# Optimization experiments

Hardware: AMD Instinct MI355X
Metric: run time of the kernel (lower is better)

The kernel has to match this reference:

```python
import jax, jax.numpy as jnp
import numpy as np

B, S, D = 8, 2048, 768

def setup_inputs() -> dict:
    key = jax.random.key(0)
    kx, kq, kk, kv = jax.random.split(key, 4)
    scale = 1.0 / np.sqrt(D)
    x = jax.random.normal(kx, (B, S, D), dtype=jnp.float32)
    # nn.Linear weights: [out, in], applied as x @ W.T
    Wq = jax.random.normal(kq, (D, D), dtype=jnp.float32) * scale
    Wk = jax.random.normal(kk, (D, D), dtype=jnp.float32) * scale
    Wv = jax.random.normal(kv, (D, D), dtype=jnp.float32) * scale
    return {"x": x, "Wq": Wq, "Wk": Wk, "Wv": Wv}

def reference(x, Wq, Wk, Wv):
    d_k = x.shape[-1]
    Q = jnp.einsum('bsd,ed->bse', x, Wq)
    K = jnp.einsum('bsd,ed->bse', x, Wk)
    V = jnp.einsum('bsd,ed->bse', x, Wv)
    scores = jnp.einsum('bqd,bkd->bqk', Q, K) / jnp.sqrt(jnp.float32(d_k))
    attention_weights = jax.nn.softmax(scores, axis=-1)  # [B,S,S]
    weighted_values = jnp.einsum('bqk,bkd->bqd', attention_weights, V)
    return (weighted_values, attention_weights)
```

## Files before the change

kernel.cpp:

```cpp
#include <hip/hip_runtime.h>
#include <cmath>


typedef __bf16 v8bf __attribute__((ext_vector_type(8)));
typedef float  v4f  __attribute__((ext_vector_type(4)));
typedef unsigned short u16;

__device__ __forceinline__ u16 f2bf(float f) {
  union { float f; unsigned u; } v; v.f = f;
  unsigned r = v.u + 0x7fffu + ((v.u >> 16) & 1u);
  return (u16)(r >> 16);
}

__device__ __forceinline__ uint4 pack8(const float* __restrict__ src) {
  float4 f0 = *(const float4*)src;
  float4 f1 = *(const float4*)(src + 4);
  union { uint4 u; u16 h[8]; } pk;
  pk.h[0] = f2bf(f0.x); pk.h[1] = f2bf(f0.y); pk.h[2] = f2bf(f0.z); pk.h[3] = f2bf(f0.w);
  pk.h[4] = f2bf(f1.x); pk.h[5] = f2bf(f1.y); pk.h[6] = f2bf(f1.z); pk.h[7] = f2bf(f1.w);
  return pk.u;
}

__device__ __forceinline__ void gl_lds16(const void* g, void* l) {
  __builtin_amdgcn_global_load_lds(
      (const __attribute__((address_space(1))) unsigned*)g,
      (__attribute__((address_space(3))) unsigned*)l, 16, 0, 0);
}

enum { OUT_F32 = 0, OUT_BF16 = 1, OUT_VT_BF16 = 2 };

constexpr int BM = 128, BN = 128, BK = 64;

template <bool A_F32, int MODE>
__global__ __launch_bounds__(256)
void gemm128(const void* __restrict__ Ag_, const void* __restrict__ Bg_,
             void* __restrict__ Cg, int K, int lda, int ldb, int ldc,
             long long sA, long long sB, long long sC, float alpha) {
  __shared__ u16 As[BM * BK];
  __shared__ u16 Bs[BN * BK];

  const int z  = blockIdx.z;
  const int m0 = blockIdx.x * BM;
  const int n0 = blockIdx.y * BN;

  const int t    = threadIdx.x;
  const int lane = t & 63;
  const int w    = t >> 6;
  const int wm   = (w & 1) * 64;
  const int wn   = (w >> 1) * 64;
  const int fr   = lane & 15;
  const int quad = lane >> 4;

  const u16* Bp = (const u16*)Bg_ + (size_t)z * (size_t)sB;

  v4f acc[4][4];
#pragma unroll
  for (int i = 0; i < 4; ++i)
#pragma unroll
    for (int j = 0; j < 4; ++j) acc[i][j] = (v4f){0.f, 0.f, 0.f, 0.f};

  for (int kt = 0; kt < K; kt += BK) {
#pragma unroll
    for (int j = 0; j < 4; ++j) {
      const int s   = (w * 4 + j) * 64 + lane;
      const int row = s >> 3;
      const int gc  = (s & 7) ^ (row & 7);
      gl_lds16(Bp + (size_t)(n0 + row) * ldb + kt + gc * 8, &Bs[s * 8]);
    }
    if constexpr (A_F32) {
      const float* Ap = (const float*)Ag_ + (size_t)z * (size_t)sA;
#pragma unroll
      for (int j = 0; j < 4; ++j) {
        const int g   = j * 256 + t;
        const int row = g >> 3, gc = g & 7;
        const int s   = (g & ~7) | (gc ^ (row & 7));
        uint4 pk = pack8(Ap + (size_t)(m0 + row) * lda + kt + gc * 8);
        *(uint4*)&As[s * 8] = pk;
      }
    } else {
      const u16* Ap = (const u16*)Ag_ + (size_t)z * (size_t)sA;
#pragma unroll
      for (int j = 0; j < 4; ++j) {
        const int s   = (w * 4 + j) * 64 + lane;
        const int row = s >> 3;
        const int gc  = (s & 7) ^ (row & 7);
        gl_lds16(Ap + (size_t)(m0 + row) * lda + kt + gc * 8, &As[s * 8]);
      }
    }
    __syncthreads();

#pragma unroll
    for (int kk = 0; kk < BK; kk += 32) {
      const int kc = (kk >> 3) + quad;
      v8bf af[4], bv[4];
#pragma unroll
      for (int i = 0; i < 4; ++i) {
        const int ra = wm + i * 16 + fr;
        const int rb = wn + i * 16 + fr;
        af[i] = *(const v8bf*)&As[(ra * 8 + (kc ^ (fr & 7))) * 8];
        bv[i] = *(const v8bf*)&Bs[(rb * 8 + (kc ^ (fr & 7))) * 8];
      }
#pragma unroll
      for (int mi = 0; mi < 4; ++mi)
#pragma unroll
        for (int ni = 0; ni < 4; ++ni)
          acc[mi][ni] =
              __builtin_amdgcn_mfma_f32_16x16x32_bf16(af[mi], bv[ni], acc[mi][ni], 0, 0, 0);
    }
    __syncthreads();
  }

  const int r0 = (lane >> 4) * 4;
#pragma unroll
  for (int mi = 0; mi < 4; ++mi) {
#pragma unroll
    for (int ni = 0; ni < 4; ++ni) {
      v4f v = acc[mi][ni];
      const int grow0 = m0 + wm + mi * 16 + r0;
      const int gcol  = n0 + wn + ni * 16 + fr;
      if constexpr (MODE == OUT_F32) {
        float* C = (float*)Cg + (size_t)z * (size_t)sC;
#pragma unroll
        for (int r = 0; r < 4; ++r)
          C[(size_t)(grow0 + r) * ldc + gcol] = v[r] * alpha;
      } else if constexpr (MODE == OUT_BF16) {
        u16* C = (u16*)Cg;
#pragma unroll
        for (int r = 0; r < 4; ++r)
          C[(size_t)(grow0 + r) * ldc + gcol] = f2bf(v[r]);
      } else {
        u16* C = (u16*)Cg;
        size_t base = (size_t)(grow0 >> 11) * (768ull * 2048ull) +
                      (size_t)gcol * 2048ull + (size_t)(grow0 & 2047);
        ushort4 st;
        st.x = f2bf(v[0]); st.y = f2bf(v[1]); st.z = f2bf(v[2]); st.w = f2bf(v[3]);
        *(ushort4*)&C[base] = st;
      }
    }
  }
}

__global__ __launch_bounds__(256)
void cvt_bf16(const float* __restrict__ src, u16* __restrict__ dst, int n8) {
  const int i = blockIdx.x * 256 + threadIdx.x;
  if (i < n8) *(uint4*)(dst + (size_t)i * 8) = pack8(src + (size_t)i * 8);
}

__global__ __launch_bounds__(256)
void cvt3_bf16(const float* __restrict__ s0, const float* __restrict__ s1,
               const float* __restrict__ s2, u16* __restrict__ d0,
               u16* __restrict__ d1, u16* __restrict__ d2, int n8) {
  const float* s = blockIdx.y == 0 ? s0 : blockIdx.y == 1 ? s1 : s2;
  u16*         d = blockIdx.y == 0 ? d0 : blockIdx.y == 1 ? d1 : d2;
  const int i = blockIdx.x * 256 + threadIdx.x;
  if (i < n8) *(uint4*)(d + (size_t)i * 8) = pack8(s + (size_t)i * 8);
}

template <bool EMIT>
__global__ __launch_bounds__(256) void softmax_rows(float* __restrict__ w,
                                                    u16* __restrict__ pb) {
  float* p = w + (size_t)blockIdx.x * 2048;
  const int t = threadIdx.x;
  float4 a = *(float4*)(p + t * 4);
  float4 b = *(float4*)(p + 1024 + t * 4);

  float mx = fmaxf(fmaxf(fmaxf(a.x, a.y), fmaxf(a.z, a.w)),
                   fmaxf(fmaxf(b.x, b.y), fmaxf(b.z, b.w)));
#pragma unroll
  for (int off = 32; off; off >>= 1) mx = fmaxf(mx, __shfl_xor(mx, off));
  __shared__ float red[4];
  const int wid = t >> 6, ln = t & 63;
  if (ln == 0) red[wid] = mx;
  __syncthreads();
  mx = fmaxf(fmaxf(red[0], red[1]), fmaxf(red[2], red[3]));

  a.x = __expf(a.x - mx); a.y = __expf(a.y - mx);
  a.z = __expf(a.z - mx); a.w = __expf(a.w - mx);
  b.x = __expf(b.x - mx); b.y = __expf(b.y - mx);
  b.z = __expf(b.z - mx); b.w = __expf(b.w - mx);

  float s = a.x + a.y + a.z + a.w + b.x + b.y + b.z + b.w;
#pragma unroll
  for (int off = 32; off; off >>= 1) s += __shfl_xor(s, off);
  __syncthreads();
  if (ln == 0) red[wid] = s;
  __syncthreads();
  s = red[0] + red[1] + red[2] + red[3];

  const float inv = 1.0f / s;
  a.x *= inv; a.y *= inv; a.z *= inv; a.w *= inv;
  b.x *= inv; b.y *= inv; b.z *= inv; b.w *= inv;
  *(float4*)(p + t * 4) = a;
  *(float4*)(p + 1024 + t * 4) = b;

  if constexpr (EMIT) {
    u16* q = pb + (size_t)blockIdx.x * 2048;
    ushort4 ha, hb;
    ha.x = f2bf(a.x); ha.y = f2bf(a.y); ha.z = f2bf(a.z); ha.w = f2bf(a.w);
    hb.x = f2bf(b.x); hb.y = f2bf(b.y); hb.z = f2bf(b.z); hb.w = f2bf(b.w);
    *(ushort4*)(q + t * 4) = ha;
    *(ushort4*)(q + 1024 + t * 4) = hb;
  }
}

extern "C" void kernel_launch(void* const* d_in, const int* in_sizes, int n_in,
                              void* d_out, int out_size, void* d_ws, size_t ws_size,
                              hipStream_t stream) {
  const float* x  = (const float*)d_in[0];
  const float* Wq = (const float*)d_in[1];
  const float* Wk = (const float*)d_in[2];
  const float* Wv = (const float*)d_in[3];
  float* out = (float*)d_out;
  float* wts = out + 8ull * 2048 * 768;

  u16* Qb  = (u16*)d_out;
  u16* Kb  = Qb + 16384ull * 768;
  u16* xb  = (u16*)wts;
  u16* Wqb = xb + 16384ull * 768;
  u16* Wkb = Wqb + 768ull * 768;
  u16* Wvb = Wkb + 768ull * 768;
  u16* Vt  = (u16*)d_ws;
  u16* Pb  = Vt + 8ull * 768 * 2048;

  const size_t VT_BYTES = 8ull * 768 * 2048 * 2;
  const size_t PB_BYTES = 8ull * 2048 * 2048 * 2;
  const bool   pb_ok    = ws_size >= VT_BYTES + PB_BYTES;

  const dim3 blk(256, 1, 1);
  const float isq = 1.0f / sqrtf(768.0f);

  cvt_bf16<<<dim3(6144, 1, 1), blk, 0, stream>>>(x, xb, 16384 * 768 / 8);
  cvt3_bf16<<<dim3(288, 3, 1), blk, 0, stream>>>(Wq, Wk, Wv, Wqb, Wkb, Wvb,
                                                 768 * 768 / 8);

  gemm128<false, OUT_BF16><<<dim3(128, 6, 1), blk, 0, stream>>>(
      xb, Wqb, (void*)Qb, 768, 768, 768, 768, 0, 0, 0, 1.0f);
  gemm128<false, OUT_BF16><<<dim3(128, 6, 1), blk, 0, stream>>>(
      xb, Wkb, (void*)Kb, 768, 768, 768, 768, 0, 0, 0, 1.0f);
  gemm128<false, OUT_VT_BF16><<<dim3(128, 6, 1), blk, 0, stream>>>(
      xb, Wvb, (void*)Vt, 768, 768, 768, 0, 0, 0, 0, 1.0f);

  gemm128<false, OUT_F32><<<dim3(16, 16, 8), blk, 0, stream>>>(
      Qb, Kb, (void*)wts, 768, 768, 768, 2048,
      2048ll * 768, 2048ll * 768, 2048ll * 2048, isq);

  if (pb_ok) {
    softmax_rows<true><<<dim3(16384, 1, 1), blk, 0, stream>>>(wts, Pb);
    gemm128<false, OUT_F32><<<dim3(16, 6, 8), blk, 0, stream>>>(
        Pb, Vt, (void*)out, 2048, 2048, 2048, 768,
        2048ll * 2048, 768ll * 2048, 2048ll * 768, 1.0f);
  } else {
    softmax_rows<false><<<dim3(16384, 1, 1), blk, 0, stream>>>(wts, nullptr);
    gemm128<true, OUT_F32><<<dim3(16, 6, 8), blk, 0, stream>>>(
        wts, Vt, (void*)out, 2048, 2048, 2048, 768,
        2048ll * 2048, 768ll * 2048, 2048ll * 768, 1.0f);
  }
}
```

Before: 462.1 us.

## Add 256x256 MFMA GEMM kernel and fuse Q/K/V projections into one launch

Adds a 512-thread GEMM kernel with 256x256 tiles, a 64-wide K step, XOR-swizzled LDS staging via global_load_lds, and a workgroup-index remap that groups blocks in strides of eight. The three projection GEMMs become a single launch over the contiguous Wq/Wk/Wv bf16 buffers, with the epilogue routing each column group to Q, K or the transposed V layout. The QK^T score GEMM also moves to the larger tile. The aim is more data reuse per block and fewer launches, at the cost of higher register and LDS pressure, no double buffering, and fewer blocks in flight.

```diff
diff --git a/kernel.cpp b/kernel.cpp
--- a/kernel.cpp
+++ b/kernel.cpp
@@ -140,6 +140,130 @@
   }
 }
 
+enum { S_F32 = 0, S_QKV = 1 };
+constexpr int BM2 = 256, BN2 = 256, BK2 = 64;
+
+template <int MODE>
+__global__ __launch_bounds__(512, 2)
+void gemm256(const u16* __restrict__ Ag, const u16* __restrict__ Bg,
+             void* __restrict__ C0, void* __restrict__ C1, void* __restrict__ C2,
+             int K, int lda, int ldb, int ldc,
+             long long sA, long long sB, long long sC, float alpha) {
+  __shared__ u16 As[BM2 * BK2];
+  __shared__ u16 Bs[BN2 * BK2];
+
+  const int gx = gridDim.x, gy = gridDim.y, gz = gridDim.z;
+  const int nwg = gx * gy * gz;
+  int lid = blockIdx.x + gx * (blockIdx.y + gy * blockIdx.z);
+  if ((nwg & 7) == 0) {
+    const int cpx = nwg >> 3;
+    lid = (lid & 7) * cpx + (lid >> 3);
+  }
+  const int bx = lid % gx;
+  const int byz = lid / gx;
+  const int by = byz % gy;
+  const int z  = byz / gy;
+
+  const int m0 = bx * BM2;
+  const int n0 = by * BN2;
+
+  const int t    = threadIdx.x;
+  const int lane = t & 63;
+  const int w    = t >> 6;
+  const int wm   = (w >> 2) * 128;
+  const int wn   = (w & 3) * 64;
+  const int fr   = lane & 15;
+  const int quad = lane >> 4;
+
+  const u16* Ap = Ag + (size_t)z * (size_t)sA;
+  const u16* Bp = Bg + (size_t)z * (size_t)sB;
+
+  v4f acc[8][4];
+#pragma unroll
+  for (int i = 0; i < 8; ++i)
+#pragma unroll
+    for (int j = 0; j < 4; ++j) acc[i][j] = (v4f){0.f, 0.f, 0.f, 0.f};
+
+  for (int kt = 0; kt < K; kt += BK2) {
+#pragma unroll
+    for (int j = 0; j < 4; ++j) {
+      const int s   = (w * 4 + j) * 64 + lane;
+      const int row = s >> 3;
+      const int gc  = (s & 7) ^ (row & 7);
+      gl_lds16(Bp + (size_t)(n0 + row) * ldb + kt + gc * 8, &Bs[s * 8]);
+    }
+#pragma unroll
+    for (int j = 0; j < 4; ++j) {
+      const int s   = (w * 4 + j) * 64 + lane;
+      const int row = s >> 3;
+      const int gc  = (s & 7) ^ (row & 7);
+      gl_lds16(Ap + (size_t)(m0 + row) * lda + kt + gc * 8, &As[s * 8]);
+    }
+    __syncthreads();
+
+#pragma unroll
+    for (int kk = 0; kk < BK2; kk += 32) {
+      const int kc = (kk >> 3) + quad;
+      v8bf af[8], bv[4];
+#pragma unroll
+      for (int i = 0; i < 8; ++i) {
+        const int ra = wm + i * 16 + fr;
+        af[i] = *(const v8bf*)&As[(ra * 8 + (kc ^ (fr & 7))) * 8];
+      }
+#pragma unroll
+      for (int i = 0; i < 4; ++i) {
+        const int rb = wn + i * 16 + fr;
+        bv[i] = *(const v8bf*)&Bs[(rb * 8 + (kc ^ (fr & 7))) * 8];
+      }
+#pragma unroll
+      for (int mi = 0; mi < 8; ++mi)
+#pragma unroll
+        for (int ni = 0; ni < 4; ++ni)
+          acc[mi][ni] =
+              __builtin_amdgcn_mfma_f32_16x16x32_bf16(af[mi], bv[ni], acc[mi][ni], 0, 0, 0);
+    }
+    __syncthreads();
+  }
+
+  const int r0 = (lane >> 4) * 4;
+#pragma unroll
+  for (int mi = 0; mi < 8; ++mi) {
+#pragma unroll
+    for (int ni = 0; ni < 4; ++ni) {
+      v4f v = acc[mi][ni];
+      const int grow0 = m0 + wm + mi * 16 + r0;
+      const int gcol  = n0 + wn + ni * 16 + fr;
+      if constexpr (MODE == S_F32) {
+        float* C = (float*)C0 + (size_t)z * (size_t)sC;
+#pragma unroll
+        for (int r = 0; r < 4; ++r)
+          C[(size_t)(grow0 + r) * ldc + gcol] = v[r] * alpha;
+      } else {
+        const int grp  = n0 / 768;
+        const int lcol = gcol - grp * 768;
+        if (grp == 0) {
+          u16* C = (u16*)C0;
+#pragma unroll
+          for (int r = 0; r < 4; ++r)
+            C[(size_t)(grow0 + r) * 768 + lcol] = f2bf(v[r]);
+        } else if (grp == 1) {
+          u16* C = (u16*)C1;
+#pragma unroll
+          for (int r = 0; r < 4; ++r)
+            C[(size_t)(grow0 + r) * 768 + lcol] = f2bf(v[r]);
+        } else {
+          u16* C = (u16*)C2;
+          size_t base = (size_t)(grow0 >> 11) * (768ull * 2048ull) +
+                        (size_t)lcol * 2048ull + (size_t)(grow0 & 2047);
+          ushort4 st;
+          st.x = f2bf(v[0]); st.y = f2bf(v[1]); st.z = f2bf(v[2]); st.w = f2bf(v[3]);
+          *(ushort4*)&C[base] = st;
+        }
+      }
+    }
+  }
+}
+
 __global__ __launch_bounds__(256)
 void cvt_bf16(const float* __restrict__ src, u16* __restrict__ dst, int n8) {
   const int i = blockIdx.x * 256 + threadIdx.x;
@@ -227,21 +351,18 @@
   const bool   pb_ok    = ws_size >= VT_BYTES + PB_BYTES;
 
   const dim3 blk(256, 1, 1);
+  const dim3 blk512(512, 1, 1);
   const float isq = 1.0f / sqrtf(768.0f);
 
   cvt_bf16<<<dim3(6144, 1, 1), blk, 0, stream>>>(x, xb, 16384 * 768 / 8);
   cvt3_bf16<<<dim3(288, 3, 1), blk, 0, stream>>>(Wq, Wk, Wv, Wqb, Wkb, Wvb,
                                                  768 * 768 / 8);
 
-  gemm128<false, OUT_BF16><<<dim3(128, 6, 1), blk, 0, stream>>>(
-      xb, Wqb, (void*)Qb, 768, 768, 768, 768, 0, 0, 0, 1.0f);
-  gemm128<false, OUT_BF16><<<dim3(128, 6, 1), blk, 0, stream>>>(
-      xb, Wkb, (void*)Kb, 768, 768, 768, 768, 0, 0, 0, 1.0f);
-  gemm128<false, OUT_VT_BF16><<<dim3(128, 6, 1), blk, 0, stream>>>(
-      xb, Wvb, (void*)Vt, 768, 768, 768, 0, 0, 0, 0, 1.0f);
-
-  gemm128<false, OUT_F32><<<dim3(16, 16, 8), blk, 0, stream>>>(
-      Qb, Kb, (void*)wts, 768, 768, 768, 2048,
+  gemm256<S_QKV><<<dim3(64, 9, 1), blk512, 0, stream>>>(
+      xb, Wqb, (void*)Qb, (void*)Kb, (void*)Vt, 768, 768, 768, 0, 0, 0, 0, 1.0f);
+
+  gemm256<S_F32><<<dim3(8, 8, 8), blk512, 0, stream>>>(
+      Qb, Kb, (void*)wts, nullptr, nullptr, 768, 768, 768, 2048,
       2048ll * 768, 2048ll * 768, 2048ll * 2048, isq);
 
   if (pb_ok) {
```

Measured after the change: 491.5 us. 6.4% more time.

## Double-buffer GEMM LDS tiles and fuse Q/K/V projections into one launch

Applied to the files above, without the earlier changes.

The GEMM kernel now keeps two LDS buffers for the A and B tiles. It issues the global-to-LDS loads for the next K tile before running the MFMA work on the current one, so memory latency overlaps with compute and one barrier per iteration is dropped. The three projection GEMMs become a single launch with 18 column-block groups. It relies on the bf16 Wq/Wk/Wv buffers being contiguous and routes each group's output to Q, K or transposed V. The cost is double the LDS per block, which may reduce occupancy, and some branching in the epilogue.

```diff
diff --git a/kernel.cpp b/kernel.cpp
--- a/kernel.cpp
+++ b/kernel.cpp
@@ -27,17 +27,19 @@
       (__attribute__((address_space(3))) unsigned*)l, 16, 0, 0);
 }
 
-enum { OUT_F32 = 0, OUT_BF16 = 1, OUT_VT_BF16 = 2 };
+enum { OUT_F32 = 0, OUT_QKV = 1 };
 
 constexpr int BM = 128, BN = 128, BK = 64;
+constexpr int TILE = BM * BK;
 
 template <bool A_F32, int MODE>
 __global__ __launch_bounds__(256)
 void gemm128(const void* __restrict__ Ag_, const void* __restrict__ Bg_,
-             void* __restrict__ Cg, int K, int lda, int ldb, int ldc,
+             void* __restrict__ C0, void* __restrict__ C1, void* __restrict__ C2,
+             int K, int lda, int ldb, int ldc,
              long long sA, long long sB, long long sC, float alpha) {
-  __shared__ u16 As[BM * BK];
-  __shared__ u16 Bs[BN * BK];
+  __shared__ u16 As[2 * TILE];
+  __shared__ u16 Bs[2 * TILE];
 
   const int z  = blockIdx.z;
   const int m0 = blockIdx.x * BM;
@@ -59,13 +61,14 @@
 #pragma unroll
     for (int j = 0; j < 4; ++j) acc[i][j] = (v4f){0.f, 0.f, 0.f, 0.f};
 
-  for (int kt = 0; kt < K; kt += BK) {
+  auto stage = [&](int kt, int buf) {
 #pragma unroll
     for (int j = 0; j < 4; ++j) {
       const int s   = (w * 4 + j) * 64 + lane;
       const int row = s >> 3;
       const int gc  = (s & 7) ^ (row & 7);
-      gl_lds16(Bp + (size_t)(n0 + row) * ldb + kt + gc * 8, &Bs[s * 8]);
+      gl_lds16(Bp + (size_t)(n0 + row) * ldb + kt + gc * 8,
+               &Bs[buf * TILE + s * 8]);
     }
     if constexpr (A_F32) {
       const float* Ap = (const float*)Ag_ + (size_t)z * (size_t)sA;
@@ -75,7 +78,7 @@
         const int row = g >> 3, gc = g & 7;
         const int s   = (g & ~7) | (gc ^ (row & 7));
         uint4 pk = pack8(Ap + (size_t)(m0 + row) * lda + kt + gc * 8);
-        *(uint4*)&As[s * 8] = pk;
+        *(uint4*)&As[buf * TILE + s * 8] = pk;
       }
     } else {
       const u16* Ap = (const u16*)Ag_ + (size_t)z * (size_t)sA;
@@ -84,11 +87,21 @@
         const int s   = (w * 4 + j) * 64 + lane;
         const int row = s >> 3;
         const int gc  = (s & 7) ^ (row & 7);
-        gl_lds16(Ap + (size_t)(m0 + row) * lda + kt + gc * 8, &As[s * 8]);
-      }
-    }
-    __syncthreads();
-
+        gl_lds16(Ap + (size_t)(m0 + row) * lda + kt + gc * 8,
+                 &As[buf * TILE + s * 8]);
+      }
+    }
+  };
+
+  stage(0, 0);
+  __syncthreads();
+
+  int cur = 0;
+  for (int kt = 0; kt < K; kt += BK) {
+    if (kt + BK < K) stage(kt + BK, cur ^ 1);
+
+    const u16* Ab = &As[cur * TILE];
+    const u16* Bb = &Bs[cur * TILE];
 #pragma unroll
     for (int kk = 0; kk < BK; kk += 32) {
       const int kc = (kk >> 3) + quad;
@@ -97,8 +110,8 @@
       for (int i = 0; i < 4; ++i) {
         const int ra = wm + i * 16 + fr;
         const int rb = wn + i * 16 + fr;
-        af[i] = *(const v8bf*)&As[(ra * 8 + (kc ^ (fr & 7))) * 8];
-        bv[i] = *(const v8bf*)&Bs[(rb * 8 + (kc ^ (fr & 7))) * 8];
+        af[i] = *(const v8bf*)&Ab[(ra * 8 + (kc ^ (fr & 7))) * 8];
+        bv[i] = *(const v8bf*)&Bb[(rb * 8 + (kc ^ (fr & 7))) * 8];
       }
 #pragma unroll
       for (int mi = 0; mi < 4; ++mi)
@@ -108,6 +121,7 @@
               __builtin_amdgcn_mfma_f32_16x16x32_bf16(af[mi], bv[ni], acc[mi][ni], 0, 0, 0);
     }
     __syncthreads();
+    cur ^= 1;
   }
 
   const int r0 = (lane >> 4) * 4;
@@ -119,22 +133,31 @@
       const int grow0 = m0 + wm + mi * 16 + r0;
       const int gcol  = n0 + wn + ni * 16 + fr;
       if constexpr (MODE == OUT_F32) {
-        float* C = (float*)Cg + (size_t)z * (size_t)sC;
+        float* C = (float*)C0 + (size_t)z * (size_t)sC;
 #pragma unroll
         for (int r = 0; r < 4; ++r)
           C[(size_t)(grow0 + r) * ldc + gcol] = v[r] * alpha;
-      } else if constexpr (MODE == OUT_BF16) {
-        u16* C = (u16*)Cg;
-#pragma unroll
-        for (int r = 0; r < 4; ++r)
-          C[(size_t)(grow0 + r) * ldc + gcol] = f2bf(v[r]);
       } else {
-        u16* C = (u16*)Cg;
-        size_t base = (size_t)(grow0 >> 11) * (768ull * 2048ull) +
-                      (size_t)gcol * 2048ull + (size_t)(grow0 & 2047);
-        ushort4 st;
-        st.x = f2bf(v[0]); st.y = f2bf(v[1]); st.z = f2bf(v[2]); st.w = f2bf(v[3]);
-        *(ushort4*)&C[base] = st;
+        const int grp  = n0 / 768;
+        const int lcol = (n0 - grp * 768) + wn + ni * 16 + fr;
+        if (grp == 0) {
+          u16* C = (u16*)C0;
+#pragma unroll
+          for (int r = 0; r < 4; ++r)
+            C[(size_t)(grow0 + r) * 768 + lcol] = f2bf(v[r]);
+        } else if (grp == 1) {
+          u16* C = (u16*)C1;
+#pragma unroll
+          for (int r = 0; r < 4; ++r)
+            C[(size_t)(grow0 + r) * 768 + lcol] = f2bf(v[r]);
+        } else {
+          u16* C = (u16*)C2;
+          size_t base = (size_t)(grow0 >> 11) * (768ull * 2048ull) +
+                        (size_t)lcol * 2048ull + (size_t)(grow0 & 2047);
+          ushort4 st;
+          st.x = f2bf(v[0]); st.y = f2bf(v[1]); st.z = f2bf(v[2]); st.w = f2bf(v[3]);
+          *(ushort4*)&C[base] = st;
+        }
       }
     }
   }
@@ -233,26 +256,23 @@
   cvt3_bf16<<<dim3(288, 3, 1), blk, 0, stream>>>(Wq, Wk, Wv, Wqb, Wkb, Wvb,
                                                  768 * 768 / 8);
 
-  gemm128<false, OUT_BF16><<<dim3(128, 6, 1), blk, 0, stream>>>(
-      xb, Wqb, (void*)Qb, 768, 768, 768, 768, 0, 0, 0, 1.0f);
-  gemm128<false, OUT_BF16><<<dim3(128, 6, 1), blk, 0, stream>>>(
-      xb, Wkb, (void*)Kb, 768, 768, 768, 768, 0, 0, 0, 1.0f);
-  gemm128<false, OUT_VT_BF16><<<dim3(128, 6, 1), blk, 0, stream>>>(
-      xb, Wvb, (void*)Vt, 768, 768, 768, 0, 0, 0, 0, 1.0f);
+  gemm128<false, OUT_QKV><<<dim3(128, 18, 1), blk, 0, stream>>>(
+      xb, Wqb, (void*)Qb, (void*)Kb, (void*)Vt, 768, 768, 768, 768,
+      0, 0, 0, 1.0f);
 
   gemm128<false, OUT_F32><<<dim3(16, 16, 8), blk, 0, stream>>>(
-      Qb, Kb, (void*)wts, 768, 768, 768, 2048,
+      Qb, Kb, (void*)wts, nullptr, nullptr, 768, 768, 768, 2048,
       2048ll * 768, 2048ll * 768, 2048ll * 2048, isq);
 
   if (pb_ok) {
     softmax_rows<true><<<dim3(16384, 1, 1), blk, 0, stream>>>(wts, Pb);
     gemm128<false, OUT_F32><<<dim3(16, 6, 8), blk, 0, stream>>>(
-        Pb, Vt, (void*)out, 2048, 2048, 2048, 768,
+        Pb, Vt, (void*)out, nullptr, nullptr, 2048, 2048, 2048, 768,
         2048ll * 2048, 768ll * 2048, 2048ll * 768, 1.0f);
   } else {
     softmax_rows<false><<<dim3(16384, 1, 1), blk, 0, stream>>>(wts, nullptr);
     gemm128<true, OUT_F32><<<dim3(16, 6, 8), blk, 0, stream>>>(
-        wts, Vt, (void*)out, 2048, 2048, 2048, 768,
+        wts, Vt, (void*)out, nullptr, nullptr, 2048, 2048, 2048, 768,
         2048ll * 2048, 768ll * 2048, 2048ll * 768, 1.0f);
   }
 }
```

Measured after the change: 493.3 us. 1.07x slower.
